# Kernel tuning notes

Measured on AMD Instinct MI355X. Metric: run time of the kernel, lower is better.

## Reference

```python
import jax, jax.numpy as jnp
import numpy as np

B, H, W = 16, 512, 512
N_BINS = 511          # round(mean(shape)) - 1 for (512, 512)
MAX_R = 1.0           # (1 + min(shape)/max(shape)) / 2 for square image


def _bin_ids():
    # Precompute per-pixel radial shell index (replaces the list of boolean shell masks).
    frame = max(H, W)
    xx, yy = np.mgrid[:H, :W]
    ellipse = ((xx - H / 2) * 2 / frame) ** 2 + ((yy - W / 2) * 2 / frame) ** 2
    r2 = np.linspace(0.0, MAX_R, N_BINS + 1)[1:] ** 2
    # shell k = { r2[k-1] <= ellipse < r2[k] }; pixels with ellipse >= r2[-1] map to
    # overflow bin N_BINS and are dropped, exactly matching the xor'd ellipse masks.
    return jnp.asarray(np.searchsorted(r2, ellipse.ravel(), side='right').astype(np.int32))


BIN_IDS = _bin_ids()  # [H*W] int32 in [0, N_BINS]


def setup_inputs() -> dict:
    key = jax.random.key(0)
    k1, k2 = jax.random.split(key)
    return {
        "z_": jax.random.normal(k1, (B, H, W, 2), dtype=jnp.float32),
        "t_": jax.random.normal(k2, (B, H, W, 2), dtype=jnp.float32),
    }


def _shell_sums(x):
    # x: [B, H*W] -> per-shell sums [B, N_BINS+1] in a single fused segment-sum pass.
    return jax.vmap(lambda v: jax.ops.segment_sum(v, BIN_IDS, num_segments=N_BINS + 1))(x)


def reference(z_, t_):
    tc = t_[..., 0] + 1j * t_[..., 1]          # [B,H,W] complex target
    zc = z_[..., 0] + 1j * z_[..., 1]
    Ft = jnp.fft.fft2(tc, axes=(-2, -1))
    Fe = jnp.fft.fft2(zc - tc, axes=(-2, -1))
    norm_coeff = Ft.real ** 2 + Ft.imag ** 2   # |FFT(target)|^2, [B,H,W]
    errors = Fe.real ** 2 + Fe.imag ** 2       # |FFT(z - target)|^2
    es = _shell_sums(errors.reshape(B, -1))[:, :N_BINS]      # drop overflow bin
    ns = _shell_sums(norm_coeff.reshape(B, -1))[:, :N_BINS]
    nre = es / jnp.maximum(ns, 1e-8)           # per-batch, per-shell normed error
    # per_shell_loss = per-batch sum over shells; loss = mean over batch
    return jnp.mean(jnp.sum(nre, axis=1))
```

## Files before the change

### kernel.cpp

```cpp
#include <hip/hip_runtime.h>

#define HH 512
#define WW 512
#define NBATCH 16
#define NBINS 512
#define NCG 64

#define PI_F 3.14159265358979323846f

#define SW(r) ((r) ^ (((r) >> 4) & 0xF))

__device__ __forceinline__ float2 cadd(float2 a, float2 b){ return make_float2(a.x+b.x, a.y+b.y); }
__device__ __forceinline__ float2 csub(float2 a, float2 b){ return make_float2(a.x-b.x, a.y-b.y); }
__device__ __forceinline__ float2 cmul(float2 a, float2 b){
    return make_float2(a.x*b.x - a.y*b.y, a.x*b.y + a.y*b.x);
}

__device__ __forceinline__ void dft8(const float2* a, float2* y) {
    const float s2 = 0.70710678118654752440f;
    float2 t02a = cadd(a[0], a[4]), t02s = csub(a[0], a[4]);
    float2 t13a = cadd(a[2], a[6]), t13s = csub(a[2], a[6]);
    float2 E0 = cadd(t02a, t13a);
    float2 E2 = csub(t02a, t13a);
    float2 E1 = make_float2(t02s.x + t13s.y, t02s.y - t13s.x);
    float2 E3 = make_float2(t02s.x - t13s.y, t02s.y + t13s.x);
    float2 u02a = cadd(a[1], a[5]), u02s = csub(a[1], a[5]);
    float2 u13a = cadd(a[3], a[7]), u13s = csub(a[3], a[7]);
    float2 O0 = cadd(u02a, u13a);
    float2 O2 = csub(u02a, u13a);
    float2 O1 = make_float2(u02s.x + u13s.y, u02s.y - u13s.x);
    float2 O3 = make_float2(u02s.x - u13s.y, u02s.y + u13s.x);
    float2 wO1 = make_float2(s2 * (O1.x + O1.y), s2 * (O1.y - O1.x));
    float2 wO2 = make_float2(O2.y, -O2.x);
    float2 wO3 = make_float2(s2 * (O3.y - O3.x), -s2 * (O3.x + O3.y));
    y[0] = cadd(E0, O0);  y[4] = csub(E0, O0);
    y[1] = cadd(E1, wO1); y[5] = csub(E1, wO1);
    y[2] = cadd(E2, wO2); y[6] = csub(E2, wO2);
    y[3] = cadd(E3, wO3); y[7] = csub(E3, wO3);
}

__device__ __forceinline__ void twiddle8(float base, float2* w) {
    float s1, c1, s4, c4;
    __sincosf(base, &s1, &c1);
    __sincosf(4.0f * base, &s4, &c4);
    w[0] = make_float2(1.0f, 0.0f);
    w[1] = make_float2(c1, s1);
    w[2] = cmul(w[1], w[1]);
    w[3] = cmul(w[2], w[1]);
    w[4] = make_float2(c4, s4);
    w[5] = cmul(w[4], w[1]);
    w[6] = cmul(w[4], w[2]);
    w[7] = cmul(w[4], w[3]);
}

__device__ __forceinline__ void fft512_stage0_store(float2* rb, int lane, const float2* a) {
    float2 y[8]; dft8(a, y);
    float2 w[8]; twiddle8(-PI_F * (float)lane * (1.0f / 256.0f), w);
#pragma unroll
    for (int r = 0; r < 8; ++r) rb[SW(8 * lane + r)] = cmul(y[r], w[r]);
}

__device__ __forceinline__ void fft512_stage1(float2* rb, int lane) {
    float2 a[8];
#pragma unroll
    for (int u = 0; u < 8; ++u) a[u] = rb[SW(lane + 64 * u)];
    float2 y[8]; dft8(a, y);
    float2 w[8]; twiddle8(-PI_F * (float)(lane >> 3) * (1.0f / 32.0f), w);
    const int qb = (lane & 7) + ((lane >> 3) << 6);
#pragma unroll
    for (int r = 0; r < 8; ++r) rb[SW(qb + 8 * r)] = cmul(y[r], w[r]);
}

__device__ __forceinline__ void fft512_stage2(const float2* rb, int lane, float2* y) {
    float2 a[8];
#pragma unroll
    for (int u = 0; u < 8; ++u) a[u] = rb[SW(lane + 64 * u)];
    dft8(a, y);
}

__global__ __launch_bounds__(256, 4)
void row_fft_kernel(const float2* __restrict__ z, const float2* __restrict__ t,
                    float2* __restrict__ fields, int b0) {
    __shared__ float2 buf[4 * 512];
    const int tid  = threadIdx.x;
    const int lane = tid & 63;
    const int g    = tid >> 6;
    const int bid  = blockIdx.x;
    const int lb   = bid >> 8;
    const int h    = ((bid & 255) << 1) | (g >> 1);
    const int f    = g & 1;
    const int b    = b0 + lb;
    const size_t rowOff = ((size_t)(b * HH + h)) * WW;

    float2 a[8];
    if (f == 0) {
        const float2* tr = t + rowOff;
#pragma unroll
        for (int u = 0; u < 8; ++u) a[u] = tr[lane + 64 * u];
    } else {
        const float2* tr = t + rowOff;
        const float2* zr = z + rowOff;
#pragma unroll
        for (int u = 0; u < 8; ++u) {
            float2 tv = tr[lane + 64 * u];
            float2 zv = zr[lane + 64 * u];
            a[u] = make_float2(zv.x - tv.x, zv.y - tv.y);
        }
    }
    float2* rb = buf + (g << 9);
    fft512_stage0_store(rb, lane, a);
    __builtin_amdgcn_wave_barrier();
    fft512_stage1(rb, lane);
    __builtin_amdgcn_wave_barrier();
    float2 y[8];
    fft512_stage2(rb, lane, y);

    float2* orow = fields + ((size_t)(lb * 2 + f) * HH + h) * WW;
#pragma unroll
    for (int r = 0; r < 8; ++r) orow[lane + 64 * r] = y[r];
}

__global__ __launch_bounds__(512, 4)
void col_fft_bin_kernel(const float2* __restrict__ fields,
                        float* __restrict__ partials, int b0) {
    __shared__ float2 colBuf[8 * 512];
    __shared__ float hist[NBINS];
    const int tid  = threadIdx.x;
    const int lane = tid & 63;
    const int g    = tid >> 6;
    const int bid  = blockIdx.x;
    const int cg   = bid & 63;
    const int fl   = bid >> 6;
    const int f    = fl & 1;
    const int b    = b0 + (fl >> 1);
    const int c0   = cg << 3;

    const float4* src4 = (const float4*)(fields + (size_t)fl * (HH * WW) + c0);
#pragma unroll
    for (int k = 0; k < 4; ++k) {
        int p  = tid + (k << 9);
        int i  = p >> 2;
        int jj = p & 3;
        float4 v = src4[(size_t)i * (WW / 2) + jj];
        colBuf[((2 * jj)     << 9) + SW(i)] = make_float2(v.x, v.y);
        colBuf[((2 * jj + 1) << 9) + SW(i)] = make_float2(v.z, v.w);
    }
    hist[tid] = 0.0f;
    __syncthreads();

    float2* rb = colBuf + (g << 9);
    {
        float2 a[8];
#pragma unroll
        for (int u = 0; u < 8; ++u) a[u] = rb[SW(lane + 64 * u)];
        fft512_stage0_store(rb, lane, a);
    }
    __builtin_amdgcn_wave_barrier();
    fft512_stage1(rb, lane);
    __builtin_amdgcn_wave_barrier();
    float2 y[8];
    fft512_stage2(rb, lane, y);

    const int c = c0 + g;
    const float fcv = (float)(c - 256) * (1.0f / 256.0f);
    const float fc2 = fcv * fcv;
#pragma unroll
    for (int r = 0; r < 8; ++r) {
        int k = lane + (r << 6);
        float fr = (float)(k - 256) * (1.0f / 256.0f);
        float e = fr * fr + fc2;
        int bin = min((int)(sqrt((double)e) * 511.0), 511);
        float mag = y[r].x * y[r].x + y[r].y * y[r].y;
        atomicAdd(&hist[bin], mag);
    }
    __syncthreads();

    partials[(((size_t)f * NBATCH + b) * NCG + cg) * NBINS + tid] = hist[tid];
}

__global__ __launch_bounds__(512)
void loss_kernel(const float* __restrict__ partials, float* __restrict__ outp) {
    __shared__ float red[512];
    const int b = blockIdx.x;
    const int tid = threadIdx.x;
    float ns = 0.0f, es = 0.0f;
    const float* pn = partials + ((size_t)(0 * NBATCH + b) * NCG) * NBINS + tid;
    const float* pe = partials + ((size_t)(1 * NBATCH + b) * NCG) * NBINS + tid;
#pragma unroll 4
    for (int cgi = 0; cgi < NCG; ++cgi) {
        ns += pn[cgi * NBINS];
        es += pe[cgi * NBINS];
    }
    red[tid] = (tid < 511) ? es / fmaxf(ns, 1e-8f) : 0.0f;
    __syncthreads();
    for (int s = 256; s > 0; s >>= 1) {
        if (tid < s) red[tid] += red[tid + s];
        __syncthreads();
    }
    if (tid == 0) atomicAdd(outp, red[0] * (1.0f / NBATCH));
}

extern "C" void kernel_launch(void* const* d_in, const int* in_sizes, int n_in,
                              void* d_out, int out_size, void* d_ws, size_t ws_size,
                              hipStream_t stream) {
    const float2* z = (const float2*)d_in[0];
    const float2* t = (const float2*)d_in[1];
    float* outp = (float*)d_out;

    const size_t partBytes = (size_t)2 * NBATCH * NCG * NBINS * sizeof(float);
    const size_t fpb = (size_t)2 * HH * WW * sizeof(float2);

    int CB = 16;
    while (CB > 1 && partBytes + (size_t)CB * fpb > ws_size) CB >>= 1;

    float*  partials = (float*)d_ws;
    float2* fields   = (float2*)((char*)d_ws + partBytes);

    hipMemsetAsync(outp, 0, sizeof(float), stream);

    for (int b0 = 0; b0 < NBATCH; b0 += CB) {
        row_fft_kernel<<<CB * 256, 256, 0, stream>>>(z, t, fields, b0);
        col_fft_bin_kernel<<<CB * 2 * 64, 512, 0, stream>>>(fields, partials, b0);
    }
    loss_kernel<<<NBATCH, 512, 0, stream>>>(partials, outp);
}
```

Measured before the change: 179.6 us.

## Store row-FFT output transposed and accumulate shell bins with global atomics

The row FFT kernel now processes 8 rows per block, computing both the target and the error FFT from a single read of each row. It writes its output transposed through a swizzled shared-memory tile, so the column kernel can read each column contiguously instead of running a strided gather. Per-block histograms are added atomically into a compact per-batch bin array rather than a large partials buffer, which lets the loss kernel collapse into one block. The extra shared-memory transpose and the added block barriers cost something, and global atomics replace a plain partials reduction.

After: 158.2 us. -11.9%, faster.

```diff
diff --git a/kernel.cpp b/kernel.cpp
--- a/kernel.cpp
+++ b/kernel.cpp
@@ -4,11 +4,11 @@
 #define WW 512
 #define NBATCH 16
 #define NBINS 512
-#define NCG 64
 
 #define PI_F 3.14159265358979323846f
 
 #define SW(r) ((r) ^ (((r) >> 4) & 0xF))
+#define TSW(c, hh) (((c) << 3) + ((hh) ^ (((c) >> 1) & 7)))
 
 __device__ __forceinline__ float2 cadd(float2 a, float2 b){ return make_float2(a.x+b.x, a.y+b.y); }
 __device__ __forceinline__ float2 csub(float2 a, float2 b){ return make_float2(a.x-b.x, a.y-b.y); }
@@ -78,52 +78,70 @@
     dft8(a, y);
 }
 
-__global__ __launch_bounds__(256, 4)
+__global__ __launch_bounds__(512, 4)
 void row_fft_kernel(const float2* __restrict__ z, const float2* __restrict__ t,
-                    float2* __restrict__ fields, int b0) {
-    __shared__ float2 buf[4 * 512];
+                    float2* __restrict__ fieldsT, int b0) {
+    __shared__ float2 buf[8 * 512];
     const int tid  = threadIdx.x;
     const int lane = tid & 63;
     const int g    = tid >> 6;
     const int bid  = blockIdx.x;
-    const int lb   = bid >> 8;
-    const int h    = ((bid & 255) << 1) | (g >> 1);
-    const int f    = g & 1;
+    const int hg   = bid & 63;
+    const int lb   = bid >> 6;
     const int b    = b0 + lb;
+    const int h    = (hg << 3) | g;
     const size_t rowOff = ((size_t)(b * HH + h)) * WW;
 
-    float2 a[8];
-    if (f == 0) {
-        const float2* tr = t + rowOff;
-#pragma unroll
-        for (int u = 0; u < 8; ++u) a[u] = tr[lane + 64 * u];
-    } else {
-        const float2* tr = t + rowOff;
-        const float2* zr = z + rowOff;
-#pragma unroll
-        for (int u = 0; u < 8; ++u) {
-            float2 tv = tr[lane + 64 * u];
-            float2 zv = zr[lane + 64 * u];
-            a[u] = make_float2(zv.x - tv.x, zv.y - tv.y);
-        }
-    }
+    const float2* tr = t + rowOff;
+    const float2* zr = z + rowOff;
+    float2 tv[8], zv[8];
+#pragma unroll
+    for (int u = 0; u < 8; ++u) tv[u] = tr[lane + 64 * u];
+#pragma unroll
+    for (int u = 0; u < 8; ++u) zv[u] = zr[lane + 64 * u];
+
     float2* rb = buf + (g << 9);
-    fft512_stage0_store(rb, lane, a);
-    __builtin_amdgcn_wave_barrier();
-    fft512_stage1(rb, lane);
-    __builtin_amdgcn_wave_barrier();
-    float2 y[8];
-    fft512_stage2(rb, lane, y);
-
-    float2* orow = fields + ((size_t)(lb * 2 + f) * HH + h) * WW;
-#pragma unroll
-    for (int r = 0; r < 8; ++r) orow[lane + 64 * r] = y[r];
+#pragma unroll
+    for (int f = 0; f < 2; ++f) {
+        float2 a[8];
+        if (f == 0) {
+#pragma unroll
+            for (int u = 0; u < 8; ++u) a[u] = tv[u];
+        } else {
+#pragma unroll
+            for (int u = 0; u < 8; ++u) a[u] = make_float2(zv[u].x - tv[u].x,
+                                                           zv[u].y - tv[u].y);
+        }
+        fft512_stage0_store(rb, lane, a);
+        __builtin_amdgcn_wave_barrier();
+        fft512_stage1(rb, lane);
+        __builtin_amdgcn_wave_barrier();
+        float2 y[8];
+        fft512_stage2(rb, lane, y);
+
+        __syncthreads();
+#pragma unroll
+        for (int r = 0; r < 8; ++r) {
+            int c = lane + (r << 6);
+            buf[TSW(c, g)] = y[r];
+        }
+        __syncthreads();
+        float2* outF = fieldsT + ((size_t)(lb * 2 + f) << 18);
+#pragma unroll
+        for (int k = 0; k < 8; ++k) {
+            int e  = tid + (k << 9);
+            int c  = e >> 3;
+            int hh = e & 7;
+            outF[((size_t)c << 9) + (hg << 3) + hh] = buf[TSW(c, hh)];
+        }
+        __syncthreads();
+    }
 }
 
 __global__ __launch_bounds__(512, 4)
-void col_fft_bin_kernel(const float2* __restrict__ fields,
-                        float* __restrict__ partials, int b0) {
-    __shared__ float2 colBuf[8 * 512];
+void col_fft_bin_kernel(const float2* __restrict__ fieldsT,
+                        float* __restrict__ bins, int b0) {
+    __shared__ float2 buf[8 * 512];
     __shared__ float hist[NBINS];
     const int tid  = threadIdx.x;
     const int lane = tid & 63;
@@ -133,35 +151,24 @@
     const int fl   = bid >> 6;
     const int f    = fl & 1;
     const int b    = b0 + (fl >> 1);
-    const int c0   = cg << 3;
-
-    const float4* src4 = (const float4*)(fields + (size_t)fl * (HH * WW) + c0);
-#pragma unroll
-    for (int k = 0; k < 4; ++k) {
-        int p  = tid + (k << 9);
-        int i  = p >> 2;
-        int jj = p & 3;
-        float4 v = src4[(size_t)i * (WW / 2) + jj];
-        colBuf[((2 * jj)     << 9) + SW(i)] = make_float2(v.x, v.y);
-        colBuf[((2 * jj + 1) << 9) + SW(i)] = make_float2(v.z, v.w);
-    }
+    const int c    = (cg << 3) | g;
+
     hist[tid] = 0.0f;
     __syncthreads();
 
-    float2* rb = colBuf + (g << 9);
-    {
-        float2 a[8];
-#pragma unroll
-        for (int u = 0; u < 8; ++u) a[u] = rb[SW(lane + 64 * u)];
-        fft512_stage0_store(rb, lane, a);
-    }
+    const float2* colT = fieldsT + (((size_t)fl << 9) + c) * 512;
+    float2 a[8];
+#pragma unroll
+    for (int u = 0; u < 8; ++u) a[u] = colT[lane + (u << 6)];
+
+    float2* rb = buf + (g << 9);
+    fft512_stage0_store(rb, lane, a);
     __builtin_amdgcn_wave_barrier();
     fft512_stage1(rb, lane);
     __builtin_amdgcn_wave_barrier();
     float2 y[8];
     fft512_stage2(rb, lane, y);
 
-    const int c = c0 + g;
     const float fcv = (float)(c - 256) * (1.0f / 256.0f);
     const float fc2 = fcv * fcv;
 #pragma unroll
@@ -169,35 +176,35 @@
         int k = lane + (r << 6);
         float fr = (float)(k - 256) * (1.0f / 256.0f);
         float e = fr * fr + fc2;
-        int bin = min((int)(sqrt((double)e) * 511.0), 511);
-        float mag = y[r].x * y[r].x + y[r].y * y[r].y;
-        atomicAdd(&hist[bin], mag);
+        if (e < 1.0f) {
+            int bin = (int)(sqrt((double)e) * 511.0);
+            atomicAdd(&hist[bin], y[r].x * y[r].x + y[r].y * y[r].y);
+        }
     }
     __syncthreads();
-
-    partials[(((size_t)f * NBATCH + b) * NCG + cg) * NBINS + tid] = hist[tid];
+    atomicAdd(&bins[((size_t)f * NBATCH + b) * NBINS + tid], hist[tid]);
 }
 
 __global__ __launch_bounds__(512)
-void loss_kernel(const float* __restrict__ partials, float* __restrict__ outp) {
+void loss_kernel(const float* __restrict__ bins, float* __restrict__ outp) {
     __shared__ float red[512];
-    const int b = blockIdx.x;
     const int tid = threadIdx.x;
-    float ns = 0.0f, es = 0.0f;
-    const float* pn = partials + ((size_t)(0 * NBATCH + b) * NCG) * NBINS + tid;
-    const float* pe = partials + ((size_t)(1 * NBATCH + b) * NCG) * NBINS + tid;
+    float acc = 0.0f;
+    if (tid < 511) {
 #pragma unroll 4
-    for (int cgi = 0; cgi < NCG; ++cgi) {
-        ns += pn[cgi * NBINS];
-        es += pe[cgi * NBINS];
-    }
-    red[tid] = (tid < 511) ? es / fmaxf(ns, 1e-8f) : 0.0f;
+        for (int b = 0; b < NBATCH; ++b) {
+            float ns = bins[((size_t)b) * NBINS + tid];
+            float es = bins[((size_t)(NBATCH + b)) * NBINS + tid];
+            acc += es / fmaxf(ns, 1e-8f);
+        }
+    }
+    red[tid] = acc;
     __syncthreads();
     for (int s = 256; s > 0; s >>= 1) {
         if (tid < s) red[tid] += red[tid + s];
         __syncthreads();
     }
-    if (tid == 0) atomicAdd(outp, red[0] * (1.0f / NBATCH));
+    if (tid == 0) outp[0] = red[0] * (1.0f / NBATCH);
 }
 
 extern "C" void kernel_launch(void* const* d_in, const int* in_sizes, int n_in,
@@ -207,20 +214,20 @@
     const float2* t = (const float2*)d_in[1];
     float* outp = (float*)d_out;
 
-    const size_t partBytes = (size_t)2 * NBATCH * NCG * NBINS * sizeof(float);
+    const size_t binsBytes = (size_t)2 * NBATCH * NBINS * sizeof(float);
     const size_t fpb = (size_t)2 * HH * WW * sizeof(float2);
 
     int CB = 16;
-    while (CB > 1 && partBytes + (size_t)CB * fpb > ws_size) CB >>= 1;
-
-    float*  partials = (float*)d_ws;
-    float2* fields   = (float2*)((char*)d_ws + partBytes);
-
-    hipMemsetAsync(outp, 0, sizeof(float), stream);
+    while (CB > 1 && binsBytes + (size_t)CB * fpb > ws_size) CB >>= 1;
+
+    float*  bins    = (float*)d_ws;
+    float2* fieldsT = (float2*)((char*)d_ws + binsBytes);
+
+    hipMemsetAsync(bins, 0, binsBytes, stream);
 
     for (int b0 = 0; b0 < NBATCH; b0 += CB) {
-        row_fft_kernel<<<CB * 256, 256, 0, stream>>>(z, t, fields, b0);
-        col_fft_bin_kernel<<<CB * 2 * 64, 512, 0, stream>>>(fields, partials, b0);
-    }
-    loss_kernel<<<NBATCH, 512, 0, stream>>>(partials, outp);
-}
+        row_fft_kernel<<<CB * 64, 512, 0, stream>>>(z, t, fieldsT, b0);
+        col_fft_bin_kernel<<<CB * 2 * 64, 512, 0, stream>>>(fieldsT, bins, b0);
+    }
+    loss_kernel<<<1, 512, 0, stream>>>(bins, outp);
+}
```
